# Kernel tuning notes

Measured on AMD Instinct MI355X. Metric: run time of the kernel, lower is better.

The kernel has to match this reference:

```python
import jax, jax.numpy as jnp
import numpy as np

EPS = 1e-5

def _bn(x, g, b):
    m = x.mean(axis=0)
    v = x.var(axis=0)  # biased, matches torch BN training normalization
    return g * (x - m) * jax.lax.rsqrt(v + EPS) + b

def _mlp(x, W1, b1, g1, be1, W2, b2, g2, be2):
    h = jax.nn.relu(_bn(x @ W1 + b1, g1, be1))
    return jax.nn.relu(_bn(h @ W2 + b2, g2, be2))

def setup_inputs() -> dict:
    key = jax.random.key(0)
    ks = jax.random.split(key, 12)
    n, e, d, de = 100000, 1600000, 128, 16
    def lin(k, fan_in, fan_out):
        bound = 1.0 / np.sqrt(fan_in)
        k1, k2 = jax.random.split(k)
        W = jax.random.uniform(k1, (fan_in, fan_out), jnp.float32, -bound, bound)
        b = jax.random.uniform(k2, (fan_out,), jnp.float32, -bound, bound)
        return W, b
    msg_W1, msg_b1 = lin(ks[0], 2 * d + de, d)
    msg_W2, msg_b2 = lin(ks[1], d, d)
    upd_W1, upd_b1 = lin(ks[2], 3 * d, d)
    upd_W2, upd_b2 = lin(ks[3], d, d)
    return {
        "h": jax.random.normal(ks[4], (n, d), jnp.float32),
        "edge_index": jax.random.randint(ks[5], (2, e), 0, n, jnp.int64),
        "edge_attr": jax.random.normal(ks[6], (e, de), jnp.float32),
        "msg_W1": msg_W1, "msg_b1": msg_b1,
        "msg_g1": jnp.ones((d,)), "msg_be1": jnp.zeros((d,)),
        "msg_W2": msg_W2, "msg_b2": msg_b2,
        "msg_g2": jnp.ones((d,)), "msg_be2": jnp.zeros((d,)),
        "upd_W1": upd_W1, "upd_b1": upd_b1,
        "upd_g1": jnp.ones((d,)), "upd_be1": jnp.zeros((d,)),
        "upd_W2": upd_W2, "upd_b2": upd_b2,
        "upd_g2": jnp.ones((d,)), "upd_be2": jnp.zeros((d,)),
    }

def reference(h, edge_index, edge_attr,
              msg_W1, msg_b1, msg_g1, msg_be1, msg_W2, msg_b2, msg_g2, msg_be2,
              upd_W1, upd_b1, upd_g1, upd_be1, upd_W2, upd_b2, upd_g2, upd_be2):
    alpha = 0.5
    n = h.shape[0]
    src = edge_index[0]
    dst = edge_index[1]
    h_i = h[src]  # (e, d)
    h_j = h[dst]  # (e, d)
    msg_args = (msg_W1, msg_b1, msg_g1, msg_be1, msg_W2, msg_b2, msg_g2, msg_be2)
    m_st = _mlp(jnp.concatenate([h_i, h_j, edge_attr], axis=-1), *msg_args)
    m_ts = _mlp(jnp.concatenate([h_j, h_i, edge_attr], axis=-1), *msg_args)
    # NOTE: original code scatters both directions by source nodes (faithful)
    a_st = jax.ops.segment_sum(m_st, src, num_segments=n)
    a_ts = jax.ops.segment_sum(m_ts, src, num_segments=n)
    upd_in = jnp.concatenate([h, alpha * a_st, (1.0 - alpha) * a_ts], axis=-1)
    return _mlp(upd_in, upd_W1, upd_b1, upd_g1, upd_be1, upd_W2, upd_b2, upd_g2, upd_be2)
```

## Files before the change

kernel.cpp:

```cpp
#include <hip/hip_runtime.h>

#define EPS_BN 1e-5f

typedef __bf16 bf16x8 __attribute__((ext_vector_type(8)));
typedef float f32x4 __attribute__((ext_vector_type(4)));
typedef unsigned short us8 __attribute__((ext_vector_type(8)));
typedef unsigned short us4 __attribute__((ext_vector_type(4)));
typedef unsigned int u32x4 __attribute__((ext_vector_type(4)));

__device__ __forceinline__ unsigned short f2bf(float x) {
  unsigned u = __builtin_bit_cast(unsigned, x);
  unsigned r = (u + 0x7fffu + ((u >> 16) & 1u)) >> 16;
  return (unsigned short)r;
}
__device__ __forceinline__ unsigned pack2bf(float a, float b) {
  return (unsigned)f2bf(a) | ((unsigned)f2bf(b) << 16);
}
__device__ __forceinline__ unsigned long long pack4bf(float a, float b, float c, float d) {
  return (unsigned long long)pack2bf(a, b) | ((unsigned long long)pack2bf(c, d) << 32);
}
__device__ __forceinline__ float ubf(unsigned short u) {
  return __builtin_bit_cast(float, (unsigned)u << 16);
}

__device__ __forceinline__ int fragidx(int k, int c) {
  int nf = c >> 4, lr = c & 15, ks = k >> 5, lq = (k >> 3) & 3, j = k & 7;
  return ((((nf << 2) + ks) << 6) | (lq << 4) | lr) * 8 + j;
}

__global__ __launch_bounds__(256) void prep_all(
    const float* __restrict__ mW1, const float* __restrict__ mW2,
    const float* __restrict__ uW1, const float* __restrict__ uW2,
    unsigned short* __restrict__ wfrag) {
  int b = blockIdx.x;
  const float* src;
  float sc = 1.f;
  switch (b) {
    case 0: src = mW1; break;
    case 1: src = mW1 + 16384; break;
    case 2: src = mW2; break;
    case 3: src = uW1; break;
    case 4: src = uW1 + 16384; sc = 0.5f; break;
    case 5: src = uW1 + 32768; sc = 0.5f; break;
    default: src = uW2; break;
  }
  unsigned short* oc = wfrag + (long)b * 16384;
  for (int i = threadIdx.x; i < 16384; i += 256) {
    oc[fragidx(i >> 7, i & 127)] = f2bf(src[i] * sc);
  }
}

__global__ __launch_bounds__(256) void hist_kernel(
    const int* __restrict__ SRC, long E, int* __restrict__ counts) {
  long i = (long)blockIdx.x * 256 + threadIdx.x;
  long str = (long)gridDim.x * 256;
  for (; i < E; i += str) atomicAdd(&counts[SRC[i]], 1);
}

__global__ __launch_bounds__(256) void scan1(
    const int* __restrict__ counts, int n, int* __restrict__ tmp,
    int* __restrict__ bsum) {
  __shared__ int sd[256];
  int b = blockIdx.x, tid = threadIdx.x;
  int base = b * 1024 + tid * 4;
  int c[4], t = 0;
  #pragma unroll
  for (int j = 0; j < 4; ++j) {
    int idx = base + j;
    c[j] = (idx < n) ? counts[idx] : 0;
    t += c[j];
  }
  sd[tid] = t;
  __syncthreads();
  for (int off = 1; off < 256; off <<= 1) {
    int v = (tid >= off) ? sd[tid - off] : 0;
    __syncthreads();
    sd[tid] += v;
    __syncthreads();
  }
  int run = sd[tid] - t;
  #pragma unroll
  for (int j = 0; j < 4; ++j) {
    int idx = base + j;
    if (idx < n) tmp[idx] = run;
    run += c[j];
  }
  if (tid == 255) bsum[b] = sd[255];
}

__global__ __launch_bounds__(256) void scan2(int* __restrict__ bsum, int nb) {
  __shared__ int sd[256];
  int tid = threadIdx.x;
  int v = (tid < nb) ? bsum[tid] : 0;
  sd[tid] = v;
  __syncthreads();
  for (int off = 1; off < 256; off <<= 1) {
    int x = (tid >= off) ? sd[tid - off] : 0;
    __syncthreads();
    sd[tid] += x;
    __syncthreads();
  }
  if (tid < nb) bsum[tid] = sd[tid] - v;
}

__global__ __launch_bounds__(256) void scan3(
    const int* __restrict__ tmp, const int* __restrict__ bsum, int n,
    int* __restrict__ cursor) {
  int i = blockIdx.x * 256 + threadIdx.x;
  if (i < n) cursor[i] = tmp[i] + bsum[i >> 10];
}

__global__ __launch_bounds__(256) void permute_edges(
    const int* __restrict__ SRC, const int* __restrict__ DST,
    const float* __restrict__ EA, long E, int* __restrict__ cursor,
    int* __restrict__ sS, int* __restrict__ sD,
    unsigned short* __restrict__ EAb) {
  long i = (long)blockIdx.x * 256 + threadIdx.x;
  long str = (long)gridDim.x * 256;
  for (; i < E; i += str) {
    int s = SRC[i];
    int pos = atomicAdd(&cursor[s], 1);
    sS[pos] = s;
    sD[pos] = DST[i];
    const float4* ep = (const float4*)(EA + i * 16);
    float4 a = ep[0], b = ep[1], c = ep[2], d = ep[3];
    u32x4 lo, hi;
    lo[0] = pack2bf(a.x, a.y); lo[1] = pack2bf(a.z, a.w);
    lo[2] = pack2bf(b.x, b.y); lo[3] = pack2bf(b.z, b.w);
    hi[0] = pack2bf(c.x, c.y); hi[1] = pack2bf(c.z, c.w);
    hi[2] = pack2bf(d.x, d.y); hi[3] = pack2bf(d.z, d.w);
    *(u32x4*)(EAb + (long)pos * 16) = lo;
    *(u32x4*)(EAb + (long)pos * 16 + 8) = hi;
  }
}

__global__ __launch_bounds__(256) void node_mfma_pq(
    const float* __restrict__ h, const unsigned short* __restrict__ WfA,
    unsigned short* __restrict__ pqb, int n) {
  __shared__ unsigned short WT[16384];
  int tid = threadIdx.x;
  int lid = tid & 63, w = tid >> 6, lr = lid & 15, lq = lid >> 4;
  long rbase = (long)blockIdx.x * 64 + 16 * w;
  long r = rbase + lr;
  bool rv = (r < n);
  long rl = rv ? r : 0;
  const us8* WF8 = (const us8*)WT;

  bf16x8 af[4];
  const float* Ar = h + rl * 128;
  #pragma unroll
  for (int ks = 0; ks < 4; ++ks) {
    int e0 = 32 * ks + 8 * lq;
    float4 x = *(const float4*)(Ar + e0);
    float4 y = *(const float4*)(Ar + e0 + 4);
    u32x4 t;
    t[0] = pack2bf(x.x, x.y); t[1] = pack2bf(x.z, x.w);
    t[2] = pack2bf(y.x, y.y); t[3] = pack2bf(y.z, y.w);
    if (!rv) { t[0] = 0; t[1] = 0; t[2] = 0; t[3] = 0; }
    af[ks] = __builtin_bit_cast(bf16x8, t);
  }

  f32x4 accP[8], accQ[8];
  #pragma unroll
  for (int nf = 0; nf < 8; ++nf) {
    accP[nf] = f32x4{0.f, 0.f, 0.f, 0.f};
    accQ[nf] = f32x4{0.f, 0.f, 0.f, 0.f};
  }

  for (int i = tid; i < 2048; i += 256) ((us8*)WT)[i] = ((const us8*)WfA)[i];
  __syncthreads();
  #pragma unroll
  for (int nf = 0; nf < 8; ++nf) {
    #pragma unroll
    for (int ks = 0; ks < 4; ++ks) {
      bf16x8 bf = __builtin_bit_cast(bf16x8, WF8[(nf * 4 + ks) * 64 + lid]);
      accP[nf] = __builtin_amdgcn_mfma_f32_16x16x32_bf16(af[ks], bf, accP[nf], 0, 0, 0);
    }
  }
  __syncthreads();
  for (int i = tid; i < 2048; i += 256) ((us8*)WT)[i] = ((const us8*)(WfA + 16384))[i];
  __syncthreads();
  #pragma unroll
  for (int nf = 0; nf < 8; ++nf) {
    #pragma unroll
    for (int ks = 0; ks < 4; ++ks) {
      bf16x8 bf = __builtin_bit_cast(bf16x8, WF8[(nf * 4 + ks) * 64 + lid]);
      accQ[nf] = __builtin_amdgcn_mfma_f32_16x16x32_bf16(af[ks], bf, accQ[nf], 0, 0, 0);
    }
  }

  #pragma unroll
  for (int nf = 0; nf < 8; ++nf) {
    #pragma unroll
    for (int i = 0; i < 4; ++i) {
      long nd = rbase + 4 * lq + i;
      if (nd < n) {
        int ch = 16 * nf + lr;
        pqb[nd * 256 + ch] = f2bf(accP[nf][i]);
        pqb[nd * 256 + 128 + ch] = f2bf(accQ[nf][i]);
      }
    }
  }
}

template <bool ABF16>
__global__ __launch_bounds__(256) void node_mfma(
    const void* A0, const void* A1, const void* A2,
    const unsigned short* __restrict__ Wf,
    float* __restrict__ C, int n, int dostats,
    float* __restrict__ sum_out, float* __restrict__ ssq_out, int nk) {
  __shared__ unsigned short WT[16384];
  int tid = threadIdx.x;
  int lid = tid & 63, w = tid >> 6, lr = lid & 15, lq = lid >> 4;
  long rbase = (long)blockIdx.x * 64 + 16 * w;

  const void* As[3] = {A0, A1, A2};
  f32x4 acc[8];
  #pragma unroll
  for (int nf = 0; nf < 8; ++nf) acc[nf] = f32x4{0.f, 0.f, 0.f, 0.f};

  long r = rbase + lr;
  bool rv = (r < n);
  long rl = rv ? r : 0;
  const us8* WF8 = (const us8*)WT;

  for (int c = 0; c < nk; ++c) {
    if (c) __syncthreads();
    const us8* src = (const us8*)(Wf + (long)c * 16384);
    for (int i = tid; i < 2048; i += 256) ((us8*)WT)[i] = src[i];
    __syncthreads();

    bf16x8 af[4];
    if (ABF16) {
      const us8* Ar = (const us8*)((const unsigned short*)As[c] + rl * 128);
      #pragma unroll
      for (int ks = 0; ks < 4; ++ks) {
        us8 v = Ar[ks * 4 + lq];
        if (!rv) v = us8{0, 0, 0, 0, 0, 0, 0, 0};
        af[ks] = __builtin_bit_cast(bf16x8, v);
      }
    } else {
      const float* Ar = (const float*)As[c] + rl * 128;
      #pragma unroll
      for (int ks = 0; ks < 4; ++ks) {
        int e0 = 32 * ks + 8 * lq;
        float4 x = *(const float4*)(Ar + e0);
        float4 y = *(const float4*)(Ar + e0 + 4);
        u32x4 t;
        t[0] = pack2bf(x.x, x.y); t[1] = pack2bf(x.z, x.w);
        t[2] = pack2bf(y.x, y.y); t[3] = pack2bf(y.z, y.w);
        if (!rv) { t[0] = 0; t[1] = 0; t[2] = 0; t[3] = 0; }
        af[ks] = __builtin_bit_cast(bf16x8, t);
      }
    }
    #pragma unroll
    for (int nf = 0; nf < 8; ++nf) {
      #pragma unroll
      for (int ks = 0; ks < 4; ++ks) {
        bf16x8 bf = __builtin_bit_cast(bf16x8, WF8[(nf * 4 + ks) * 64 + lid]);
        acc[nf] = __builtin_amdgcn_mfma_f32_16x16x32_bf16(af[ks], bf, acc[nf], 0, 0, 0);
      }
    }
  }

  float lsum[8], lssq[8];
  #pragma unroll
  for (int nf = 0; nf < 8; ++nf) { lsum[nf] = 0.f; lssq[nf] = 0.f; }
  #pragma unroll
  for (int nf = 0; nf < 8; ++nf) {
    #pragma unroll
    for (int i = 0; i < 4; ++i) {
      long nd = rbase + 4 * lq + i;
      if (nd < n) {
        float v = acc[nf][i];
        C[nd * 128 + 16 * nf + lr] = v;
        lsum[nf] += v; lssq[nf] += v * v;
      }
    }
  }
  if (dostats) {
    #pragma unroll
    for (int nf = 0; nf < 8; ++nf) {
      float v0 = lsum[nf]; v0 += __shfl_xor(v0, 16); v0 += __shfl_xor(v0, 32);
      float v1 = lssq[nf]; v1 += __shfl_xor(v1, 16); v1 += __shfl_xor(v1, 32);
      if (lq == 0) {
        atomicAdd(&sum_out[16 * nf + lr], v0);
        atomicAdd(&ssq_out[16 * nf + lr], v1);
      }
    }
  }
}

__global__ __launch_bounds__(256) void msg_stats1b(
    const unsigned short* __restrict__ PQ,
    const unsigned short* __restrict__ EAb, const float* __restrict__ W1e,
    const int* __restrict__ SRC, const int* __restrict__ DST, long E,
    float* __restrict__ stats) {
  __shared__ float Wel[16][128];
  __shared__ float red[32][16];
  int tid = threadIdx.x;
  for (int i = tid; i < 16 * 128; i += 256) ((float*)Wel)[i] = W1e[i];
  for (int i = tid; i < 512; i += 256) ((float*)red)[i] = 0.f;
  __syncthreads();
  int c4 = tid & 31, grp = tid >> 5;
  float4 s_st = {0,0,0,0}, q_st = {0,0,0,0}, s_ts = {0,0,0,0}, q_ts = {0,0,0,0};
  long stride = (long)gridDim.x * 8;
  for (long e = (long)blockIdx.x * 8 + grp; e < E; e += stride) {
    int s = SRC[e], t = DST[e];
    const unsigned short* Rs = PQ + (long)s * 256;
    const unsigned short* Rt = PQ + (long)t * 256;
    us4 Ps = *(const us4*)(Rs + 4 * c4);
    us4 Qs = *(const us4*)(Rs + 128 + 4 * c4);
    us4 Pt = *(const us4*)(Rt + 4 * c4);
    us4 Qt = *(const us4*)(Rt + 128 + 4 * c4);
    us8 evlo = *(const us8*)(EAb + e * 16);
    us8 evhi = *(const us8*)(EAb + e * 16 + 8);
    float rx = 0.f, ry = 0.f, rz = 0.f, rw = 0.f;
    #pragma unroll
    for (int k = 0; k < 16; ++k) {
      float f = (k < 8) ? ubf(evlo[k & 7]) : ubf(evhi[k & 7]);
      const float4 w4 = *(const float4*)&Wel[k][c4 * 4];
      rx = fmaf(f, w4.x, rx); ry = fmaf(f, w4.y, ry);
      rz = fmaf(f, w4.z, rz); rw = fmaf(f, w4.w, rw);
    }
    float zx = ubf(Ps[0]) + ubf(Qt[0]) + rx, zy = ubf(Ps[1]) + ubf(Qt[1]) + ry;
    float zz = ubf(Ps[2]) + ubf(Qt[2]) + rz, zw = ubf(Ps[3]) + ubf(Qt[3]) + rw;
    s_st.x += zx; s_st.y += zy; s_st.z += zz; s_st.w += zw;
    q_st.x += zx * zx; q_st.y += zy * zy; q_st.z += zz * zz; q_st.w += zw * zw;
    float ux = ubf(Pt[0]) + ubf(Qs[0]) + rx, uy = ubf(Pt[1]) + ubf(Qs[1]) + ry;
    float uz = ubf(Pt[2]) + ubf(Qs[2]) + rz, uw = ubf(Pt[3]) + ubf(Qs[3]) + rw;
    s_ts.x += ux; s_ts.y += uy; s_ts.z += uz; s_ts.w += uw;
    q_ts.x += ux * ux; q_ts.y += uy * uy; q_ts.z += uz * uz; q_ts.w += uw * uw;
  }
  atomicAdd(&red[c4][0], s_st.x);  atomicAdd(&red[c4][1], s_st.y);
  atomicAdd(&red[c4][2], s_st.z);  atomicAdd(&red[c4][3], s_st.w);
  atomicAdd(&red[c4][4], q_st.x);  atomicAdd(&red[c4][5], q_st.y);
  atomicAdd(&red[c4][6], q_st.z);  atomicAdd(&red[c4][7], q_st.w);
  atomicAdd(&red[c4][8], s_ts.x);  atomicAdd(&red[c4][9], s_ts.y);
  atomicAdd(&red[c4][10], s_ts.z); atomicAdd(&red[c4][11], s_ts.w);
  atomicAdd(&red[c4][12], q_ts.x); atomicAdd(&red[c4][13], q_ts.y);
  atomicAdd(&red[c4][14], q_ts.z); atomicAdd(&red[c4][15], q_ts.w);
  __syncthreads();
  #pragma unroll
  for (int rep = 0; rep < 2; ++rep) {
    int j = rep * 256 + tid;
    int cc = j >> 4, k = j & 15, group = k >> 2, comp = k & 3;
    atomicAdd(&stats[group * 128 + cc * 4 + comp], red[cc][k]);
  }
}

template <bool SCATTER>
__global__ __launch_bounds__(256) void msg_mfma5(
    const unsigned short* __restrict__ PQ,
    const unsigned short* __restrict__ EAb, const float* __restrict__ W1e,
    const unsigned short* __restrict__ W2f,
    const int* __restrict__ SRC, const int* __restrict__ DST, long E,
    const float* __restrict__ sc1, const float* __restrict__ sc2,
    float* __restrict__ stats2,
    float* __restrict__ a_st, float* __restrict__ a_ts) {
  __shared__ float Wel[16][128];
  __shared__ unsigned short W2F[16384];
  __shared__ unsigned short Ast[64][136];
  __shared__ unsigned short Ats[64][136];
  __shared__ int sArr[64];

  int tid = threadIdx.x;
  int c4 = tid & 31;
  int slot = tid >> 5;
  int lid = tid & 63;
  int w = tid >> 6;
  int lr = lid & 15;
  int lq = lid >> 4;

  for (int i = tid; i < 16 * 128; i += 256) ((float*)Wel)[i] = W1e[i];
  for (int i = tid; i < 2048; i += 256) ((us8*)W2F)[i] = ((const us8*)W2f)[i];
  const us8* W2F8 = (const us8*)W2F;

  const float4* sc1v = (const float4*)sc1;
  float4 scst = sc1v[c4], shst = sc1v[32 + c4];
  float4 scts = sc1v[64 + c4], shts = sc1v[96 + c4];

  float s2st[8], h2st[8], s2ts[8], h2ts[8];
  if constexpr (SCATTER) {
    #pragma unroll
    for (int nf = 0; nf < 8; ++nf) {
      int ch = 16 * nf + lr;
      s2st[nf] = sc2[ch];       h2st[nf] = sc2[128 + ch];
      s2ts[nf] = sc2[256 + ch]; h2ts[nf] = sc2[384 + ch];
    }
  }
  float ssum_st[8], sssq_st[8], ssum_ts[8], sssq_ts[8];
  if constexpr (!SCATTER) {
    #pragma unroll
    for (int nf = 0; nf < 8; ++nf) {
      ssum_st[nf] = 0.f; sssq_st[nf] = 0.f; ssum_ts[nf] = 0.f; sssq_ts[nf] = 0.f;
    }
  }
  __syncthreads();

  for (long tb = (long)blockIdx.x * 64; tb < E; tb += (long)gridDim.x * 64) {
    int nE = (int)(E - tb < 64 ? E - tb : 64);

    #pragma unroll 2
    for (int rep = 0; rep < 8; ++rep) {
      int er = rep * 8 + slot;
      if (er < nE) {
        long e = tb + er;
        int s = SRC[e], t = DST[e];
        if (SCATTER && c4 == 0) sArr[er] = s;
        const us4* Rs = (const us4*)(PQ + (long)s * 256);
        const us4* Rt = (const us4*)(PQ + (long)t * 256);
        us4 Ps = Rs[c4];
        us4 Qs = Rs[32 + c4];
        us4 Pt = Rt[c4];
        us4 Qt = Rt[32 + c4];
        us8 evlo = *(const us8*)(EAb + e * 16);
        us8 evhi = *(const us8*)(EAb + e * 16 + 8);
        float rx = 0.f, ry = 0.f, rz = 0.f, rw = 0.f;
        #pragma unroll
        for (int k = 0; k < 16; ++k) {
          float f = (k < 8) ? ubf(evlo[k & 7]) : ubf(evhi[k & 7]);
          const float4 w4 = *(const float4*)&Wel[k][c4 * 4];
          rx = fmaf(f, w4.x, rx); ry = fmaf(f, w4.y, ry);
          rz = fmaf(f, w4.z, rz); rw = fmaf(f, w4.w, rw);
        }
        float ax = fmaxf(fmaf(ubf(Ps[0]) + ubf(Qt[0]) + rx, scst.x, shst.x), 0.f);
        float ay = fmaxf(fmaf(ubf(Ps[1]) + ubf(Qt[1]) + ry, scst.y, shst.y), 0.f);
        float az = fmaxf(fmaf(ubf(Ps[2]) + ubf(Qt[2]) + rz, scst.z, shst.z), 0.f);
        float aw = fmaxf(fmaf(ubf(Ps[3]) + ubf(Qt[3]) + rw, scst.w, shst.w), 0.f);
        *(unsigned long long*)&Ast[er][c4 * 4] = pack4bf(ax, ay, az, aw);
        float bx = fmaxf(fmaf(ubf(Pt[0]) + ubf(Qs[0]) + rx, scts.x, shts.x), 0.f);
        float by = fmaxf(fmaf(ubf(Pt[1]) + ubf(Qs[1]) + ry, scts.y, shts.y), 0.f);
        float bz = fmaxf(fmaf(ubf(Pt[2]) + ubf(Qs[2]) + rz, scts.z, shts.z), 0.f);
        float bw = fmaxf(fmaf(ubf(Pt[3]) + ubf(Qs[3]) + rw, scts.w, shts.w), 0.f);
        *(unsigned long long*)&Ats[er][c4 * 4] = pack4bf(bx, by, bz, bw);
      } else {
        *(unsigned long long*)&Ast[er][c4 * 4] = 0ull;
        *(unsigned long long*)&Ats[er][c4 * 4] = 0ull;
      }
    }
    __syncthreads();

    int arow = 16 * w + lr;
    const char* astp = (const char*)&Ast[arow][0];
    const char* atsp = (const char*)&Ats[arow][0];
    int acolb = lq * 16;
    bf16x8 afst[4], afts[4];
    #pragma unroll
    for (int ks = 0; ks < 4; ++ks) {
      afst[ks] = *(const bf16x8*)(astp + ks * 64 + acolb);
      afts[ks] = *(const bf16x8*)(atsp + ks * 64 + acolb);
    }
    int srow[4];
    if constexpr (SCATTER) {
      #pragma unroll
      for (int i = 0; i < 4; ++i) {
        int row = 16 * w + 4 * lq + i;
        srow[i] = (row < nE) ? sArr[row] : -1;
      }
    }
    #pragma unroll
    for (int nf = 0; nf < 8; ++nf) {
      f32x4 acc_st = {0.f, 0.f, 0.f, 0.f};
      f32x4 acc_ts = {0.f, 0.f, 0.f, 0.f};
      #pragma unroll
      for (int ks = 0; ks < 4; ++ks) {
        bf16x8 bf = __builtin_bit_cast(bf16x8, W2F8[(nf * 4 + ks) * 64 + lid]);
        acc_st = __builtin_amdgcn_mfma_f32_16x16x32_bf16(afst[ks], bf, acc_st, 0, 0, 0);
        acc_ts = __builtin_amdgcn_mfma_f32_16x16x32_bf16(afts[ks], bf, acc_ts, 0, 0, 0);
      }
      if constexpr (SCATTER) {
        int ch = 16 * nf + lr;
        int cur = srow[0];
        float m1 = fmaxf(fmaf(acc_st[0], s2st[nf], h2st[nf]), 0.f);
        float m2 = fmaxf(fmaf(acc_ts[0], s2ts[nf], h2ts[nf]), 0.f);
        #pragma unroll
        for (int i = 1; i < 4; ++i) {
          float v1 = fmaxf(fmaf(acc_st[i], s2st[nf], h2st[nf]), 0.f);
          float v2 = fmaxf(fmaf(acc_ts[i], s2ts[nf], h2ts[nf]), 0.f);
          if (srow[i] == cur) {
            m1 += v1; m2 += v2;
          } else {
            if (cur >= 0) {
              if (m1 != 0.f) atomicAdd(&a_st[(long)cur * 128 + ch], m1);
              if (m2 != 0.f) atomicAdd(&a_ts[(long)cur * 128 + ch], m2);
            }
            cur = srow[i]; m1 = v1; m2 = v2;
          }
        }
        if (cur >= 0) {
          if (m1 != 0.f) atomicAdd(&a_st[(long)cur * 128 + ch], m1);
          if (m2 != 0.f) atomicAdd(&a_ts[(long)cur * 128 + ch], m2);
        }
      } else {
        #pragma unroll
        for (int i = 0; i < 4; ++i) {
          ssum_st[nf] += acc_st[i]; sssq_st[nf] += acc_st[i] * acc_st[i];
          ssum_ts[nf] += acc_ts[i]; sssq_ts[nf] += acc_ts[i] * acc_ts[i];
        }
      }
    }
    __syncthreads();
  }

  if constexpr (!SCATTER) {
    #pragma unroll
    for (int nf = 0; nf < 8; ++nf) {
      float v0 = ssum_st[nf]; v0 += __shfl_xor(v0, 16); v0 += __shfl_xor(v0, 32);
      float v1 = sssq_st[nf]; v1 += __shfl_xor(v1, 16); v1 += __shfl_xor(v1, 32);
      float v2 = ssum_ts[nf]; v2 += __shfl_xor(v2, 16); v2 += __shfl_xor(v2, 32);
      float v3 = sssq_ts[nf]; v3 += __shfl_xor(v3, 16); v3 += __shfl_xor(v3, 32);
      if (lq == 0) {
        int ch = 16 * nf + lr;
        atomicAdd(&stats2[ch], v0);
        atomicAdd(&stats2[128 + ch], v1);
        atomicAdd(&stats2[256 + ch], v2);
        atomicAdd(&stats2[384 + ch], v3);
      }
    }
  }
}

__global__ void bn_finalize(const float* __restrict__ sum, const float* __restrict__ ssq,
                            float invN, const float* __restrict__ g,
                            const float* __restrict__ be,
                            float* __restrict__ sc, float* __restrict__ sh) {
  int j = threadIdx.x;
  float m = sum[j] * invN;
  float v = ssq[j] * invN - m * m;
  float s = g[j] * rsqrtf(v + EPS_BN);
  sc[j] = s;
  sh[j] = be[j] - m * s;
}

__global__ __launch_bounds__(256) void prescale_relu(
    const float* __restrict__ X, const float* __restrict__ scsh,
    unsigned* __restrict__ out, long nrows) {
  long gid = (long)blockIdx.x * 256 + threadIdx.x;
  int c2 = (int)(gid & 63);
  float s0 = scsh[2 * c2], s1 = scsh[2 * c2 + 1];
  float h0 = scsh[128 + 2 * c2], h1 = scsh[128 + 2 * c2 + 1];
  const float2* X2 = (const float2*)X;
  long rstride = ((long)gridDim.x * 256) >> 6;
  for (long row = gid >> 6; row < nrows; row += rstride) {
    float2 x = X2[row * 64 + c2];
    out[row * 64 + c2] = pack2bf(fmaxf(fmaf(x.x, s0, h0), 0.f),
                                 fmaxf(fmaf(x.y, s1, h1), 0.f));
  }
}

__global__ __launch_bounds__(256) void bn_relu_out(
    const float* __restrict__ U2, const float* __restrict__ scsh,
    float* __restrict__ out, long total) {
  long i = (long)blockIdx.x * blockDim.x + threadIdx.x;
  long stride = (long)gridDim.x * blockDim.x;
  for (; i < total; i += stride) {
    int j = (int)(i & 127);
    out[i] = fmaxf(fmaf(U2[i], scsh[j], scsh[128 + j]), 0.f);
  }
}

extern "C" void kernel_launch(void* const* d_in, const int* in_sizes, int n_in,
                              void* d_out, int out_size, void* d_ws, size_t ws_size,
                              hipStream_t stream) {
  const float* h    = (const float*)d_in[0];
  const int*   ei   = (const int*)d_in[1];
  const float* ea   = (const float*)d_in[2];
  const float* mW1  = (const float*)d_in[3];
  const float* mg1  = (const float*)d_in[5];
  const float* mbe1 = (const float*)d_in[6];
  const float* mW2  = (const float*)d_in[7];
  const float* mg2  = (const float*)d_in[9];
  const float* mbe2 = (const float*)d_in[10];
  const float* uW1  = (const float*)d_in[11];
  const float* ug1  = (const float*)d_in[13];
  const float* ube1 = (const float*)d_in[14];
  const float* uW2  = (const float*)d_in[15];
  const float* ug2  = (const float*)d_in[17];
  const float* ube2 = (const float*)d_in[18];

  int n = in_sizes[0] / 128;
  long E = (long)(in_sizes[1] / 2);
  const int* SRC = ei;
  const int* DST = ei + E;
  const float* W1e = mW1 + 256 * 128;

  size_t nf = (size_t)n * 128;
  unsigned short* pqb = (unsigned short*)d_ws;
  float* a_st = (float*)(pqb + (size_t)n * 256);
  float* a_ts = a_st + nf;
  float* st   = a_ts + nf;
  unsigned short* wfrag = (unsigned short*)(st + 3072);
  unsigned short* wfA  = wfrag;
  unsigned short* wfW2 = wfrag + 2 * 16384;
  unsigned short* wfU1 = wfrag + 3 * 16384;
  unsigned short* wfU2 = wfrag + 6 * 16384;
  int* sS = (int*)(wfrag + 7 * 16384);
  int* sD = sS + E;
  unsigned short* EAb = (unsigned short*)(sD + E);
  int* counts = (int*)(EAb + (size_t)E * 16);
  int* tmp = counts + n;
  int* bsum = tmp + n;

  float invE = 1.0f / (float)E;
  float invN = 1.0f / (float)n;
  int nblk = (n + 63) / 64;
  int nb1 = (n + 1023) / 1024;

  prep_all<<<7, 256, 0, stream>>>(mW1, mW2, uW1, uW2, wfrag);
  hipMemsetAsync(st, 0, 3072 * sizeof(float), stream);
  hipMemsetAsync(a_st, 0, 2 * nf * sizeof(float), stream);
  hipMemsetAsync(counts, 0, (size_t)n * sizeof(int), stream);

  hist_kernel<<<1024, 256, 0, stream>>>(SRC, E, counts);
  scan1<<<nb1, 256, 0, stream>>>(counts, n, tmp, bsum);
  scan2<<<1, 256, 0, stream>>>(bsum, nb1);
  scan3<<<(n + 255) / 256, 256, 0, stream>>>(tmp, bsum, n, counts);
  permute_edges<<<1024, 256, 0, stream>>>(SRC, DST, ea, E, counts, sS, sD, EAb);

  node_mfma_pq<<<nblk, 256, 0, stream>>>(h, wfA, pqb, n);

  msg_stats1b<<<2048, 256, 0, stream>>>(pqb, EAb, W1e, sS, sD, E, st);
  bn_finalize<<<1, 128, 0, stream>>>(st + 0,   st + 128, invE, mg1, mbe1, st + 1536, st + 1664);
  bn_finalize<<<1, 128, 0, stream>>>(st + 256, st + 384, invE, mg1, mbe1, st + 1792, st + 1920);

  msg_mfma5<false><<<1024, 256, 0, stream>>>(
      pqb, EAb, W1e, wfW2, sS, sD, E, st + 1536, nullptr, st + 512, nullptr, nullptr);
  bn_finalize<<<1, 128, 0, stream>>>(st + 512, st + 640, invE, mg2, mbe2, st + 2048, st + 2176);
  bn_finalize<<<1, 128, 0, stream>>>(st + 768, st + 896, invE, mg2, mbe2, st + 2304, st + 2432);

  msg_mfma5<true><<<1024, 256, 0, stream>>>(
      pqb, EAb, W1e, wfW2, sS, sD, E, st + 1536, st + 2048, nullptr, a_st, a_ts);

  float* u1 = (float*)pqb;
  node_mfma<false><<<nblk, 256, 0, stream>>>(h, a_st, a_ts, wfU1,
                                             u1, n, 1, st + 1024, st + 1152, 3);
  bn_finalize<<<1, 128, 0, stream>>>(st + 1024, st + 1152, invN, ug1, ube1, st + 2560, st + 2688);

  unsigned short* u1p = (unsigned short*)a_st;
  float* u2 = a_ts;
  prescale_relu<<<2048, 256, 0, stream>>>(u1, st + 2560, (unsigned*)u1p, n);
  node_mfma<true><<<nblk, 256, 0, stream>>>(u1p, nullptr, nullptr, wfU2,
                                            u2, n, 1, st + 1280, st + 1408, 1);
  bn_finalize<<<1, 128, 0, stream>>>(st + 1280, st + 1408, invN, ug2, ube2, st + 2816, st + 2944);

  bn_relu_out<<<2048, 256, 0, stream>>>(u2, st + 2816, (float*)d_out, (long)n * 128);
}
```

Baseline: 2.600 ms.

## Split message MFMA by direction across waves, shrink edge tile, keep edge weights in registers

The message kernel now handles 32 edges per tile instead of 64. Each wave computes only one direction (st or ts) over 16 rows, which halves MFMA accumulators and per-direction registers. The edge-attribute weights are converted to bf16 in an extra prep block and held in registers, removing the float LDS table and its reads. LDS use drops and the grid grows to 1536 blocks, aiming at higher occupancy, at the cost of more tile-loop iterations and barriers plus bf16 rounding of the edge weights.

New measurement: 2.567 ms. About the same (-1.3%).

```diff
diff --git a/kernel.cpp b/kernel.cpp
--- a/kernel.cpp
+++ b/kernel.cpp
@@ -33,6 +33,12 @@
     const float* __restrict__ uW1, const float* __restrict__ uW2,
     unsigned short* __restrict__ wfrag) {
   int b = blockIdx.x;
+  if (b == 7) {
+    const float* s7 = mW1 + 256 * 128;
+    unsigned short* oc = wfrag + 7L * 16384;
+    for (int i = threadIdx.x; i < 2048; i += 256) oc[i] = f2bf(s7[i]);
+    return;
+  }
   const float* src;
   float sc = 1.f;
   switch (b) {
@@ -350,59 +356,58 @@
 }
 
 template <bool SCATTER>
-__global__ __launch_bounds__(256) void msg_mfma5(
+__global__ __launch_bounds__(256) void msg_mfma6(
     const unsigned short* __restrict__ PQ,
-    const unsigned short* __restrict__ EAb, const float* __restrict__ W1e,
+    const unsigned short* __restrict__ EAb,
+    const unsigned short* __restrict__ Web,
     const unsigned short* __restrict__ W2f,
     const int* __restrict__ SRC, const int* __restrict__ DST, long E,
     const float* __restrict__ sc1, const float* __restrict__ sc2,
     float* __restrict__ stats2,
     float* __restrict__ a_st, float* __restrict__ a_ts) {
-  __shared__ float Wel[16][128];
   __shared__ unsigned short W2F[16384];
-  __shared__ unsigned short Ast[64][136];
-  __shared__ unsigned short Ats[64][136];
-  __shared__ int sArr[64];
+  __shared__ unsigned short Atile[2][32][136];
+  __shared__ int sArr[32];
 
   int tid = threadIdx.x;
   int c4 = tid & 31;
   int slot = tid >> 5;
-  int lid = tid & 63;
-  int w = tid >> 6;
-  int lr = lid & 15;
-  int lq = lid >> 4;
-
-  for (int i = tid; i < 16 * 128; i += 256) ((float*)Wel)[i] = W1e[i];
+  int lid = tid & 63, w = tid >> 6, lr = lid & 15, lq = lid >> 4;
+  int dir = w >> 1;
+  int half = (w & 1) * 16;
+
   for (int i = tid; i < 2048; i += 256) ((us8*)W2F)[i] = ((const us8*)W2f)[i];
   const us8* W2F8 = (const us8*)W2F;
+
+  us4 wreg[16];
+  #pragma unroll
+  for (int k = 0; k < 16; ++k) wreg[k] = *(const us4*)(Web + k * 128 + c4 * 4);
 
   const float4* sc1v = (const float4*)sc1;
   float4 scst = sc1v[c4], shst = sc1v[32 + c4];
   float4 scts = sc1v[64 + c4], shts = sc1v[96 + c4];
 
-  float s2st[8], h2st[8], s2ts[8], h2ts[8];
+  float s2[8], h2[8];
+  float ssum[8], sssq[8];
   if constexpr (SCATTER) {
+    const float* scd = sc2 + dir * 256;
     #pragma unroll
     for (int nf = 0; nf < 8; ++nf) {
       int ch = 16 * nf + lr;
-      s2st[nf] = sc2[ch];       h2st[nf] = sc2[128 + ch];
-      s2ts[nf] = sc2[256 + ch]; h2ts[nf] = sc2[384 + ch];
-    }
-  }
-  float ssum_st[8], sssq_st[8], ssum_ts[8], sssq_ts[8];
-  if constexpr (!SCATTER) {
-    #pragma unroll
-    for (int nf = 0; nf < 8; ++nf) {
-      ssum_st[nf] = 0.f; sssq_st[nf] = 0.f; ssum_ts[nf] = 0.f; sssq_ts[nf] = 0.f;
-    }
-  }
-  __syncthreads();
-
-  for (long tb = (long)blockIdx.x * 64; tb < E; tb += (long)gridDim.x * 64) {
-    int nE = (int)(E - tb < 64 ? E - tb : 64);
-
-    #pragma unroll 2
-    for (int rep = 0; rep < 8; ++rep) {
+      s2[nf] = scd[ch]; h2[nf] = scd[128 + ch];
+    }
+  } else {
+    #pragma unroll
+    for (int nf = 0; nf < 8; ++nf) { ssum[nf] = 0.f; sssq[nf] = 0.f; }
+  }
+  float* accOut = dir ? a_ts : a_st;
+  __syncthreads();
+
+  for (long tb = (long)blockIdx.x * 32; tb < E; tb += (long)gridDim.x * 32) {
+    int nE = (int)(E - tb < 32 ? E - tb : 32);
+
+    #pragma unroll
+    for (int rep = 0; rep < 4; ++rep) {
       int er = rep * 8 + slot;
       if (er < nE) {
         long e = tb + er;
@@ -420,83 +425,71 @@
         #pragma unroll
         for (int k = 0; k < 16; ++k) {
           float f = (k < 8) ? ubf(evlo[k & 7]) : ubf(evhi[k & 7]);
-          const float4 w4 = *(const float4*)&Wel[k][c4 * 4];
-          rx = fmaf(f, w4.x, rx); ry = fmaf(f, w4.y, ry);
-          rz = fmaf(f, w4.z, rz); rw = fmaf(f, w4.w, rw);
+          rx = fmaf(f, ubf(wreg[k][0]), rx);
+          ry = fmaf(f, ubf(wreg[k][1]), ry);
+          rz = fmaf(f, ubf(wreg[k][2]), rz);
+          rw = fmaf(f, ubf(wreg[k][3]), rw);
         }
         float ax = fmaxf(fmaf(ubf(Ps[0]) + ubf(Qt[0]) + rx, scst.x, shst.x), 0.f);
         float ay = fmaxf(fmaf(ubf(Ps[1]) + ubf(Qt[1]) + ry, scst.y, shst.y), 0.f);
         float az = fmaxf(fmaf(ubf(Ps[2]) + ubf(Qt[2]) + rz, scst.z, shst.z), 0.f);
         float aw = fmaxf(fmaf(ubf(Ps[3]) + ubf(Qt[3]) + rw, scst.w, shst.w), 0.f);
-        *(unsigned long long*)&Ast[er][c4 * 4] = pack4bf(ax, ay, az, aw);
+        *(unsigned long long*)&Atile[0][er][c4 * 4] = pack4bf(ax, ay, az, aw);
         float bx = fmaxf(fmaf(ubf(Pt[0]) + ubf(Qs[0]) + rx, scts.x, shts.x), 0.f);
         float by = fmaxf(fmaf(ubf(Pt[1]) + ubf(Qs[1]) + ry, scts.y, shts.y), 0.f);
         float bz = fmaxf(fmaf(ubf(Pt[2]) + ubf(Qs[2]) + rz, scts.z, shts.z), 0.f);
         float bw = fmaxf(fmaf(ubf(Pt[3]) + ubf(Qs[3]) + rw, scts.w, shts.w), 0.f);
-        *(unsigned long long*)&Ats[er][c4 * 4] = pack4bf(bx, by, bz, bw);
+        *(unsigned long long*)&Atile[1][er][c4 * 4] = pack4bf(bx, by, bz, bw);
       } else {
-        *(unsigned long long*)&Ast[er][c4 * 4] = 0ull;
-        *(unsigned long long*)&Ats[er][c4 * 4] = 0ull;
+        *(unsigned long long*)&Atile[0][er][c4 * 4] = 0ull;
+        *(unsigned long long*)&Atile[1][er][c4 * 4] = 0ull;
       }
     }
     __syncthreads();
 
-    int arow = 16 * w + lr;
-    const char* astp = (const char*)&Ast[arow][0];
-    const char* atsp = (const char*)&Ats[arow][0];
+    int arow = half + lr;
+    const char* ap = (const char*)&Atile[dir][arow][0];
     int acolb = lq * 16;
-    bf16x8 afst[4], afts[4];
+    bf16x8 af[4];
     #pragma unroll
     for (int ks = 0; ks < 4; ++ks) {
-      afst[ks] = *(const bf16x8*)(astp + ks * 64 + acolb);
-      afts[ks] = *(const bf16x8*)(atsp + ks * 64 + acolb);
+      af[ks] = *(const bf16x8*)(ap + ks * 64 + acolb);
     }
     int srow[4];
     if constexpr (SCATTER) {
       #pragma unroll
       for (int i = 0; i < 4; ++i) {
-        int row = 16 * w + 4 * lq + i;
+        int row = half + 4 * lq + i;
         srow[i] = (row < nE) ? sArr[row] : -1;
       }
     }
     #pragma unroll
     for (int nf = 0; nf < 8; ++nf) {
-      f32x4 acc_st = {0.f, 0.f, 0.f, 0.f};
-      f32x4 acc_ts = {0.f, 0.f, 0.f, 0.f};
+      f32x4 acc = {0.f, 0.f, 0.f, 0.f};
       #pragma unroll
       for (int ks = 0; ks < 4; ++ks) {
         bf16x8 bf = __builtin_bit_cast(bf16x8, W2F8[(nf * 4 + ks) * 64 + lid]);
-        acc_st = __builtin_amdgcn_mfma_f32_16x16x32_bf16(afst[ks], bf, acc_st, 0, 0, 0);
-        acc_ts = __builtin_amdgcn_mfma_f32_16x16x32_bf16(afts[ks], bf, acc_ts, 0, 0, 0);
+        acc = __builtin_amdgcn_mfma_f32_16x16x32_bf16(af[ks], bf, acc, 0, 0, 0);
       }
       if constexpr (SCATTER) {
         int ch = 16 * nf + lr;
         int cur = srow[0];
-        float m1 = fmaxf(fmaf(acc_st[0], s2st[nf], h2st[nf]), 0.f);
-        float m2 = fmaxf(fmaf(acc_ts[0], s2ts[nf], h2ts[nf]), 0.f);
+        float m = fmaxf(fmaf(acc[0], s2[nf], h2[nf]), 0.f);
         #pragma unroll
         for (int i = 1; i < 4; ++i) {
-          float v1 = fmaxf(fmaf(acc_st[i], s2st[nf], h2st[nf]), 0.f);
-          float v2 = fmaxf(fmaf(acc_ts[i], s2ts[nf], h2ts[nf]), 0.f);
+          float v = fmaxf(fmaf(acc[i], s2[nf], h2[nf]), 0.f);
           if (srow[i] == cur) {
-            m1 += v1; m2 += v2;
+            m += v;
           } else {
-            if (cur >= 0) {
-              if (m1 != 0.f) atomicAdd(&a_st[(long)cur * 128 + ch], m1);
-              if (m2 != 0.f) atomicAdd(&a_ts[(long)cur * 128 + ch], m2);
-            }
-            cur = srow[i]; m1 = v1; m2 = v2;
+            if (cur >= 0 && m != 0.f) atomicAdd(&accOut[(long)cur * 128 + ch], m);
+            cur = srow[i]; m = v;
           }
         }
-        if (cur >= 0) {
-          if (m1 != 0.f) atomicAdd(&a_st[(long)cur * 128 + ch], m1);
-          if (m2 != 0.f) atomicAdd(&a_ts[(long)cur * 128 + ch], m2);
-        }
+        if (cur >= 0 && m != 0.f) atomicAdd(&accOut[(long)cur * 128 + ch], m);
       } else {
         #pragma unroll
         for (int i = 0; i < 4; ++i) {
-          ssum_st[nf] += acc_st[i]; sssq_st[nf] += acc_st[i] * acc_st[i];
-          ssum_ts[nf] += acc_ts[i]; sssq_ts[nf] += acc_ts[i] * acc_ts[i];
+          ssum[nf] += acc[i]; sssq[nf] += acc[i] * acc[i];
         }
       }
     }
@@ -506,16 +499,12 @@
   if constexpr (!SCATTER) {
     #pragma unroll
     for (int nf = 0; nf < 8; ++nf) {
-      float v0 = ssum_st[nf]; v0 += __shfl_xor(v0, 16); v0 += __shfl_xor(v0, 32);
-      float v1 = sssq_st[nf]; v1 += __shfl_xor(v1, 16); v1 += __shfl_xor(v1, 32);
-      float v2 = ssum_ts[nf]; v2 += __shfl_xor(v2, 16); v2 += __shfl_xor(v2, 32);
-      float v3 = sssq_ts[nf]; v3 += __shfl_xor(v3, 16); v3 += __shfl_xor(v3, 32);
+      float v0 = ssum[nf]; v0 += __shfl_xor(v0, 16); v0 += __shfl_xor(v0, 32);
+      float v1 = sssq[nf]; v1 += __shfl_xor(v1, 16); v1 += __shfl_xor(v1, 32);
       if (lq == 0) {
         int ch = 16 * nf + lr;
-        atomicAdd(&stats2[ch], v0);
-        atomicAdd(&stats2[128 + ch], v1);
-        atomicAdd(&stats2[256 + ch], v2);
-        atomicAdd(&stats2[384 + ch], v3);
+        atomicAdd(&stats2[dir * 256 + ch], v0);
+        atomicAdd(&stats2[dir * 256 + 128 + ch], v1);
       }
     }
   }
@@ -595,7 +584,8 @@
   unsigned short* wfW2 = wfrag + 2 * 16384;
   unsigned short* wfU1 = wfrag + 3 * 16384;
   unsigned short* wfU2 = wfrag + 6 * 16384;
-  int* sS = (int*)(wfrag + 7 * 16384);
+  unsigned short* wfWe = wfrag + 7 * 16384;
+  int* sS = (int*)(wfWe + 2048);
   int* sD = sS + E;
   unsigned short* EAb = (unsigned short*)(sD + E);
   int* counts = (int*)(EAb + (size_t)E * 16);
@@ -607,7 +597,7 @@
   int nblk = (n + 63) / 64;
   int nb1 = (n + 1023) / 1024;
 
-  prep_all<<<7, 256, 0, stream>>>(mW1, mW2, uW1, uW2, wfrag);
+  prep_all<<<8, 256, 0, stream>>>(mW1, mW2, uW1, uW2, wfrag);
   hipMemsetAsync(st, 0, 3072 * sizeof(float), stream);
   hipMemsetAsync(a_st, 0, 2 * nf * sizeof(float), stream);
   hipMemsetAsync(counts, 0, (size_t)n * sizeof(int), stream);
@@ -624,13 +614,13 @@
   bn_finalize<<<1, 128, 0, stream>>>(st + 0,   st + 128, invE, mg1, mbe1, st + 1536, st + 1664);
   bn_finalize<<<1, 128, 0, stream>>>(st + 256, st + 384, invE, mg1, mbe1, st + 1792, st + 1920);
 
-  msg_mfma5<false><<<1024, 256, 0, stream>>>(
-      pqb, EAb, W1e, wfW2, sS, sD, E, st + 1536, nullptr, st + 512, nullptr, nullptr);
+  msg_mfma6<false><<<1536, 256, 0, stream>>>(
+      pqb, EAb, wfWe, wfW2, sS, sD, E, st + 1536, nullptr, st + 512, nullptr, nullptr);
   bn_finalize<<<1, 128, 0, stream>>>(st + 512, st + 640, invE, mg2, mbe2, st + 2048, st + 2176);
   bn_finalize<<<1, 128, 0, stream>>>(st + 768, st + 896, invE, mg2, mbe2, st + 2304, st + 2432);
 
-  msg_mfma5<true><<<1024, 256, 0, stream>>>(
-      pqb, EAb, W1e, wfW2, sS, sD, E, st + 1536, st + 2048, nullptr, a_st, a_ts);
+  msg_mfma6<true><<<1536, 256, 0, stream>>>(
+      pqb, EAb, wfWe, wfW2, sS, sD, E, st + 1536, st + 2048, nullptr, a_st, a_ts);
 
   float* u1 = (float*)pqb;
   node_mfma<false><<<nblk, 256, 0, stream>>>(h, a_st, a_ts, wfU1,
```
